# Optimization experiments

Measured on AMD Instinct MI355X. Metric: run time of the kernel, lower is better.

Reference implementation:

```python
import jax, jax.numpy as jnp
import numpy as np

D_MODEL = 1024
NUM_HEADS = 16
WINDOW = 128
DEPTH = D_MODEL // NUM_HEADS


def setup_inputs() -> dict:
    key = jax.random.key(0)
    ks = jax.random.split(key, 9)
    B, S = 2, 2048
    scale = 1.0 / np.sqrt(D_MODEL)
    x = jax.random.normal(ks[0], (B, S, D_MODEL), dtype=jnp.float32)
    Wq = jax.random.normal(ks[1], (D_MODEL, D_MODEL), dtype=jnp.float32) * scale
    Wk = jax.random.normal(ks[2], (D_MODEL, D_MODEL), dtype=jnp.float32) * scale
    Wv = jax.random.normal(ks[3], (D_MODEL, D_MODEL), dtype=jnp.float32) * scale
    Wo = jax.random.normal(ks[4], (D_MODEL, D_MODEL), dtype=jnp.float32) * scale
    bq = jnp.zeros((D_MODEL,), jnp.float32)
    bk = jnp.zeros((D_MODEL,), jnp.float32)
    bv = jnp.zeros((D_MODEL,), jnp.float32)
    bo = jnp.zeros((D_MODEL,), jnp.float32)
    return {"x": x, "Wq": Wq, "bq": bq, "Wk": Wk, "bk": bk,
            "Wv": Wv, "bv": bv, "Wo": Wo, "bo": bo}


def _split_heads(t, B, S):
    # [B,S,D] -> [B,H,S,depth]
    return t.reshape(B, S, NUM_HEADS, DEPTH).transpose(0, 2, 1, 3)


def reference(x, Wq, bq, Wk, bk, Wv, bv, Wo, bo):
    B, S, _ = x.shape
    q = _split_heads(x @ Wq + bq, B, S)
    k = _split_heads(x @ Wk + bk, B, S)
    v = _split_heads(x @ Wv + bv, B, S)
    scores = jnp.einsum('bhqd,bhkd->bhqk', q, k) / jnp.sqrt(jnp.float32(DEPTH))
    idx = jnp.arange(S)
    # mask[i_row=j, i_col=i] per original: |i - j| <= window (symmetric)
    local = jnp.abs(idx[None, :] - idx[:, None]) <= WINDOW  # [S,S]
    scores = jnp.where(local[None, None], scores, jnp.float32(-1e9))
    attn = jax.nn.softmax(scores, axis=-1)
    out = jnp.einsum('bhqk,bhkd->bhqd', attn, v)
    concat = out.transpose(0, 2, 1, 3).reshape(B, S, D_MODEL)
    return concat @ Wo + bo
```

## Files before the change

kernel.cpp:

```cpp
#include <hip/hip_runtime.h>
#include <cstdint>
#include <cstddef>

typedef __attribute__((ext_vector_type(8))) short short8;
typedef __attribute__((ext_vector_type(4))) short short4v;
typedef __attribute__((ext_vector_type(4))) float f32x4;
typedef short8 bf16x8;

typedef __attribute__((address_space(1))) const unsigned GU;
typedef __attribute__((address_space(3))) unsigned LU;

__device__ __forceinline__ short f2bf(float f) {
  unsigned u = __builtin_bit_cast(unsigned, f);
  u += 0x7fffu + ((u >> 16) & 1u);
  return (short)(u >> 16);
}

__global__ __launch_bounds__(256) void k_prep(const float* __restrict__ x,
                                              const float* __restrict__ W0, const float* __restrict__ W1,
                                              const float* __restrict__ W2, const float* __restrict__ W3,
                                              short* __restrict__ xb, short* __restrict__ WT) {
  __shared__ short T[64 * 72];
  int bid = blockIdx.x;
  int tid = threadIdx.x;
  if (bid < 2048) {
    size_t i = ((size_t)bid * 256 + tid) * 8;
    f32x4 a = *(const f32x4*)(x + i);
    f32x4 b = *(const f32x4*)(x + i + 4);
    short8 o;
#pragma unroll
    for (int j = 0; j < 4; ++j) { o[j] = f2bf(a[j]); o[4 + j] = f2bf(b[j]); }
    *(short8*)(xb + i) = o;
    return;
  }
  bid -= 2048;
  int widx = bid >> 8;
  int t = bid & 255;
  int kr = (t >> 4) * 64, nc = (t & 15) * 64;
  const float* W = widx == 0 ? W0 : widx == 1 ? W1 : widx == 2 ? W2 : W3;
  short* out = WT + (size_t)widx * 1048576;
#pragma unroll
  for (int i = 0; i < 4; ++i) {
    int idx = tid + i * 256;
    int k = idx >> 4, n4 = (idx & 15) << 2;
    f32x4 v = *(const f32x4*)(W + (size_t)(kr + k) * 1024 + nc + n4);
#pragma unroll
    for (int j = 0; j < 4; ++j) T[(n4 + j) * 72 + k] = f2bf(v[j]);
  }
  __syncthreads();
#pragma unroll
  for (int i = 0; i < 2; ++i) {
    int idx = tid + i * 256;
    int n = idx >> 3, k8 = (idx & 7) << 3;
    *(short8*)(out + (size_t)(nc + n) * 1024 + kr + k8) = *(const short8*)&T[n * 72 + k8];
  }
}

__global__ __launch_bounds__(512, 1) void k_gemm256(
    const short* __restrict__ A, const short* __restrict__ BT,
    const float* __restrict__ bias0, const float* __restrict__ bias1, const float* __restrict__ bias2,
    short* __restrict__ outb) {
  __shared__ short S[57344];
  const int tid = threadIdx.x;
  const int lane = tid & 63, w = tid >> 6;
  const int g = lane >> 4, qi = lane & 15;
  const int wm = w >> 2, wn = w & 3;
  int bid = blockIdx.x;
  int xcd = bid & 7, ii = bid >> 3;
  const int tm = (xcd >> 1) * 4 + (ii >> 3);
  const int tn = (xcd & 1) * 8 + (ii & 7);
  const int m0 = tm * 256, n0 = tn * 192;
  const size_t K = 1024;
  const short* Ab = A + (size_t)m0 * K;
  const short* Bb = BT + (size_t)n0 * K;

  auto stage64 = [&](int roff, const short* gbase, int kt) {
    int r = tid >> 3;
    int js = ((tid & 7) ^ (r & 7)) << 3;
    __builtin_amdgcn_global_load_lds((GU*)(gbase + (size_t)r * K + kt * 64 + js),
                                     (LU*)(&S[roff + tid * 8]), 16, 0, 0);
  };
  auto lda_a = [&](int bbase, int mf, int kk) -> bf16x8 {
    int row = (mf & 3) * 16 + qi;
    int reg = wm * 2 + (mf >> 2);
    return *(const bf16x8*)&S[bbase + reg * 4096 + row * 64 + (((kk * 4 + g) ^ (row & 7)) << 3)];
  };
  auto lda_b = [&](int bbase, int nf, int kk) -> bf16x8 {
    int c = wn * 48 + nf * 16 + qi;
    int reg = c >> 6, row = c & 63;
    return *(const bf16x8*)&S[bbase + 16384 + reg * 4096 + row * 64 + (((kk * 4 + g) ^ (row & 7)) << 3)];
  };

  f32x4 acc[8][3];
#pragma unroll
  for (int i = 0; i < 8; ++i)
#pragma unroll
    for (int j = 0; j < 3; ++j) acc[i][j] = (f32x4)(0.0f);

#define MFA(mi, ni, av, bv) \
  acc[mi][ni] = __builtin_amdgcn_mfma_f32_16x16x32_bf16(av, bv, acc[mi][ni], 0, 0, 0)
#define MF12(Aa, Bb_, o) \
  MFA((o)+0,0,(Aa)[(o)+0],(Bb_)[0]); MFA((o)+0,1,(Aa)[(o)+0],(Bb_)[1]); MFA((o)+0,2,(Aa)[(o)+0],(Bb_)[2]); \
  MFA((o)+1,0,(Aa)[(o)+1],(Bb_)[0]); MFA((o)+1,1,(Aa)[(o)+1],(Bb_)[1]); MFA((o)+1,2,(Aa)[(o)+1],(Bb_)[2]); \
  MFA((o)+2,0,(Aa)[(o)+2],(Bb_)[0]); MFA((o)+2,1,(Aa)[(o)+2],(Bb_)[1]); MFA((o)+2,2,(Aa)[(o)+2],(Bb_)[2]); \
  MFA((o)+3,0,(Aa)[(o)+3],(Bb_)[0]); MFA((o)+3,1,(Aa)[(o)+3],(Bb_)[1]); MFA((o)+3,2,(Aa)[(o)+3],(Bb_)[2])
#define SB __builtin_amdgcn_sched_barrier(0)
#define PHASE_TAIL(MFMAS) do { \
    SB; \
    __builtin_amdgcn_s_barrier(); \
    asm volatile("s_waitcnt lgkmcnt(0)" ::: "memory"); \
    SB; \
    __builtin_amdgcn_s_setprio(1); \
    MFMAS; \
    __builtin_amdgcn_s_setprio(0); \
    SB; \
    __builtin_amdgcn_s_barrier(); \
  } while (0)

  stage64(0,     Ab,            0);
  stage64(4096,  Ab + 65536,    0);
  stage64(8192,  Ab + 131072,   0);
  stage64(12288, Ab + 196608,   0);
  stage64(16384, Bb,            0);
  stage64(20480, Bb + 65536,    0);
  stage64(24576, Bb + 131072,   0);
  stage64(28672 + 16384, Bb,          1);
  stage64(28672 + 20480, Bb + 65536,  1);
  stage64(28672 + 24576, Bb + 131072, 1);
  asm volatile("s_waitcnt vmcnt(3)" ::: "memory");
  __builtin_amdgcn_s_barrier();

  for (int t = 0; t < 16; ++t) {
    const int b = t & 1, nb = b ^ 1;
    const int bb = b * 28672, nbb = nb * 28672;
    const int t1 = t + 1 < 15 ? t + 1 : 15;
    const int t2 = t + 2 < 15 ? t + 2 : 15;
    bf16x8 aA[8], aB[3], cA[8], cB[3];

#pragma unroll
    for (int mf = 0; mf < 4; ++mf) aA[mf] = lda_a(bb, mf, 0);
#pragma unroll
    for (int nf = 0; nf < 3; ++nf) aB[nf] = lda_b(bb, nf, 0);
    stage64(nbb,        Ab,         t1);
    stage64(nbb + 4096, Ab + 65536, t1);
    PHASE_TAIL(MF12(aA, aB, 0));
#pragma unroll
    for (int mf = 4; mf < 8; ++mf) aA[mf] = lda_a(bb, mf, 0);
#pragma unroll
    for (int nf = 0; nf < 3; ++nf) cB[nf] = lda_b(bb, nf, 1);
    stage64(nbb + 8192,  Ab + 131072, t1);
    stage64(nbb + 12288, Ab + 196608, t1);
    PHASE_TAIL(MF12(aA, aB, 4));
#pragma unroll
    for (int mf = 0; mf < 4; ++mf) cA[mf] = lda_a(bb, mf, 1);
    stage64(bb + 16384, Bb,         t2);
    stage64(bb + 20480, Bb + 65536, t2);
    PHASE_TAIL(MF12(cA, cB, 0));
#pragma unroll
    for (int mf = 4; mf < 8; ++mf) cA[mf] = lda_a(bb, mf, 1);
    stage64(bb + 24576, Bb + 131072, t2);
    asm volatile("s_waitcnt vmcnt(3)" ::: "memory");
    PHASE_TAIL(MF12(cA, cB, 4));
  }
#undef PHASE_TAIL
#undef MF12
#undef MFA
#undef SB

  asm volatile("s_waitcnt vmcnt(0)" ::: "memory");
  __syncthreads();
  float bv[3];
#pragma unroll
  for (int nf = 0; nf < 3; ++nf) {
    int colg = n0 + wn * 48 + nf * 16 + qi;
    int sel = colg >> 10;
    const float* bias = sel == 0 ? bias0 : (sel == 1 ? bias1 : bias2);
    bv[nf] = bias[colg & 1023];
  }
  short* Ep = S;
#pragma unroll
  for (int p = 0; p < 2; ++p) {
    __syncthreads();
    if (wm == p) {
#pragma unroll
      for (int mf = 0; mf < 8; ++mf)
#pragma unroll
        for (int nf = 0; nf < 3; ++nf)
#pragma unroll
          for (int j = 0; j < 4; ++j)
            Ep[(mf * 16 + g * 4 + j) * 200 + wn * 48 + nf * 16 + qi] =
                f2bf(acc[mf][nf][j] + bv[nf]);
    }
    __syncthreads();
#pragma unroll
    for (int i = 0; i < 6; ++i) {
      int idx = tid + i * 512;
      int r = idx / 24, c8 = (idx % 24) * 8;
      int grow = m0 + p * 128 + r;
      int colg = n0 + c8;
      int sel = colg >> 10;
      *(short8*)&outb[(size_t)sel * 4194304 + (size_t)grow * 1024 + (colg & 1023)] =
          *(const short8*)&Ep[r * 200 + c8];
    }
  }
}

__global__ __launch_bounds__(256, 2) void k_gemmO(
    const short* __restrict__ A, const short* __restrict__ BT,
    const float* __restrict__ bias0, float* __restrict__ outf) {
  __shared__ short Smem[16384];
  const int tid = threadIdx.x;
  const int lane = tid & 63, w = tid >> 6;
  const int g = lane >> 4, qi = lane & 15;
  const int wr = (w >> 1) * 64, wc = (w & 1) * 64;
  int bid = blockIdx.x;
  int xcd = bid & 7, ii = bid >> 3;
  const int tm = (xcd >> 1) * 8 + (ii >> 2);
  const int tn = (xcd & 1) * 4 + (ii & 3);
  const int m0 = tm * 128, n0 = tn * 128;
  const size_t K = 1024;
  const short* Ab = A + (size_t)m0 * K;
  const short* Bb = BT + (size_t)n0 * K;

  auto stage = [&](int buf, int k0) {
    short* Asb = Smem + buf * 4096;
    short* Bsb = Smem + 8192 + buf * 4096;
#pragma unroll
    for (int i = 0; i < 2; ++i) {
      int cidx = tid + i * 256;
      int r = cidx >> 2;
      int csw = ((cidx & 3) ^ ((r >> 1) & 3)) << 3;
      __builtin_amdgcn_global_load_lds((GU*)(Ab + (size_t)r * K + k0 + csw),
                                       (LU*)(&Asb[cidx * 8]), 16, 0, 0);
      __builtin_amdgcn_global_load_lds((GU*)(Bb + (size_t)r * K + k0 + csw),
                                       (LU*)(&Bsb[cidx * 8]), 16, 0, 0);
    }
  };

  f32x4 acc[4][4];
#pragma unroll
  for (int i = 0; i < 4; ++i)
#pragma unroll
    for (int j = 0; j < 4; ++j) acc[i][j] = (f32x4)(0.0f);

  stage(0, 0);
  __syncthreads();
  for (int kt = 0; kt < 32; ++kt) {
    int cur = kt & 1;
    if (kt < 31) stage(cur ^ 1, (kt + 1) * 32);
    const short* Asb = Smem + cur * 4096;
    const short* Bsb = Smem + 8192 + cur * 4096;
    bf16x8 a[4], b[4];
#pragma unroll
    for (int mf = 0; mf < 4; ++mf) {
      int R = wr + mf * 16 + qi;
      a[mf] = *(const bf16x8*)&Asb[R * 32 + ((g ^ ((R >> 1) & 3)) << 3)];
    }
#pragma unroll
    for (int nf = 0; nf < 4; ++nf) {
      int R = wc + nf * 16 + qi;
      b[nf] = *(const bf16x8*)&Bsb[R * 32 + ((g ^ ((R >> 1) & 3)) << 3)];
    }
#pragma unroll
    for (int mf = 0; mf < 4; ++mf)
#pragma unroll
      for (int nf = 0; nf < 4; ++nf)
        acc[mf][nf] = __builtin_amdgcn_mfma_f32_16x16x32_bf16(a[mf], b[nf], acc[mf][nf], 0, 0, 0);
    __syncthreads();
  }

  float* Ft = (float*)Smem;
  float bv[4];
#pragma unroll
  for (int nf = 0; nf < 4; ++nf) bv[nf] = bias0[n0 + wc + nf * 16 + qi];
#pragma unroll
  for (int mf = 0; mf < 4; ++mf) {
    __syncthreads();
#pragma unroll
    for (int nf = 0; nf < 4; ++nf)
#pragma unroll
      for (int j = 0; j < 4; ++j)
        Ft[((w >> 1) * 16 + g * 4 + j) * 136 + wc + nf * 16 + qi] = acc[mf][nf][j] + bv[nf];
    __syncthreads();
#pragma unroll
    for (int i = 0; i < 4; ++i) {
      int idx = tid + i * 256;
      int r = idx >> 5, c4 = (idx & 31) << 2;
      int row = m0 + ((r >> 4) << 6) + mf * 16 + (r & 15);
      *(f32x4*)&outf[(size_t)row * 1024 + n0 + c4] = *(const f32x4*)&Ft[r * 136 + c4];
    }
  }
}

__global__ __launch_bounds__(256, 2) void k_attn(const short* __restrict__ qg_,
                                                 const short* __restrict__ kg_,
                                                 const short* __restrict__ vg_,
                                                 short* __restrict__ outp) {
  __shared__ short Qs[64 * 72];
  __shared__ short Ks[64 * 72];
  __shared__ short Vs[64 * 72];
  __shared__ short Ps[4][16 * 72];
  int bid = blockIdx.x;
  int qt = bid & 31, h = (bid >> 5) & 15, b = bid >> 9;
  int q0 = qt * 64;
  int tid = threadIdx.x, lane = tid & 63, w = tid >> 6;
  int g = lane >> 4, qi = lane & 15;

  const short* qsrc = qg_ + ((size_t)b * 2048 + q0) * 1024 + h * 64;
#pragma unroll
  for (int i = 0; i < 2; ++i) {
    int idx = tid + i * 256;
    int r = idx >> 3, c = (idx & 7) << 3;
    *(short8*)&Qs[r * 72 + c] = *(const short8*)&qsrc[(size_t)r * 1024 + c];
  }
  __syncthreads();
  bf16x8 qf0 = *(const bf16x8*)&Qs[(w * 16 + qi) * 72 + g * 8];
  bf16x8 qf1 = *(const bf16x8*)&Qs[(w * 16 + qi) * 72 + 32 + g * 8];

  float m = -1e30f, l = 0.f;
  f32x4 oacc[4];
#pragma unroll
  for (int i = 0; i < 4; ++i) oacc[i] = (f32x4)(0.0f);
  int qglob = q0 + w * 16 + qi;

  for (int cc = 0; cc < 5; ++cc) {
    int kb0 = q0 - 128 + cc * 64;
    if (kb0 < 0 || kb0 >= 2048) continue;
    __syncthreads();
    const short* ksrc = kg_ + ((size_t)b * 2048 + kb0) * 1024 + h * 64;
    const short* vsrc = vg_ + ((size_t)b * 2048 + kb0) * 1024 + h * 64;
#pragma unroll
    for (int i = 0; i < 2; ++i) {
      int idx = tid + i * 256;
      int r = idx >> 3, c = (idx & 7) << 3;
      *(short8*)&Ks[r * 72 + c] = *(const short8*)&ksrc[(size_t)r * 1024 + c];
      short8 vv = *(const short8*)&vsrc[(size_t)r * 1024 + c];
#pragma unroll
      for (int j = 0; j < 8; ++j) {
        int d = c + j;
        Vs[d * 72 + ((r + ((d >> 3) << 3)) & 63)] = vv[j];
      }
    }
    __syncthreads();

    f32x4 st[4];
#pragma unroll
    for (int i = 0; i < 4; ++i) st[i] = (f32x4)(0.0f);
#pragma unroll
    for (int mf = 0; mf < 4; ++mf) {
      bf16x8 kf0 = *(const bf16x8*)&Ks[(mf * 16 + qi) * 72 + g * 8];
      bf16x8 kf1 = *(const bf16x8*)&Ks[(mf * 16 + qi) * 72 + 32 + g * 8];
      st[mf] = __builtin_amdgcn_mfma_f32_16x16x32_bf16(kf0, qf0, st[mf], 0, 0, 0);
      st[mf] = __builtin_amdgcn_mfma_f32_16x16x32_bf16(kf1, qf1, st[mf], 0, 0, 0);
    }

    float pv[16];
    float pm = -1e30f;
    if (cc >= 1 && cc <= 3) {
#pragma unroll
      for (int mf = 0; mf < 4; ++mf)
#pragma unroll
        for (int j = 0; j < 4; ++j) {
          float s = st[mf][j] * 0.125f;
          pv[mf * 4 + j] = s;
          pm = fmaxf(pm, s);
        }
    } else {
#pragma unroll
      for (int mf = 0; mf < 4; ++mf)
#pragma unroll
        for (int j = 0; j < 4; ++j) {
          int kcol = kb0 + mf * 16 + g * 4 + j;
          float s = st[mf][j] * 0.125f;
          int d = kcol - qglob;
          bool valid = (d >= -128) && (d <= 128);
          s = valid ? s : -1e30f;
          pv[mf * 4 + j] = s;
          pm = fmaxf(pm, s);
        }
    }
    pm = fmaxf(pm, __shfl_xor(pm, 16));
    pm = fmaxf(pm, __shfl_xor(pm, 32));
    float mnew = fmaxf(m, pm);
    float scale = __expf(m - mnew);
    float ls = 0.f;
#pragma unroll
    for (int e = 0; e < 16; ++e) {
      float p = pv[e] > -1e29f ? __expf(pv[e] - mnew) : 0.f;
      pv[e] = p;
      ls += p;
    }
    ls += __shfl_xor(ls, 16);
    ls += __shfl_xor(ls, 32);
    l = l * scale + ls;
    m = mnew;
#pragma unroll
    for (int mf = 0; mf < 4; ++mf) oacc[mf] *= scale;

#pragma unroll
    for (int f = 0; f < 4; ++f) {
      short4v pk;
#pragma unroll
      for (int j = 0; j < 4; ++j) pk[j] = f2bf(pv[f * 4 + j]);
      *(short4v*)&Ps[w][qi * 72 + f * 16 + g * 4] = pk;
    }

#pragma unroll
    for (int ks = 0; ks < 2; ++ks) {
      bf16x8 pf = *(const bf16x8*)&Ps[w][qi * 72 + ks * 32 + g * 8];
#pragma unroll
      for (int mf = 0; mf < 4; ++mf) {
        int dd = mf * 16 + qi;
        int pc = ((ks * 32 + g * 8) + ((dd >> 3) << 3)) & 63;
        bf16x8 vf = *(const bf16x8*)&Vs[dd * 72 + pc];
        oacc[mf] = __builtin_amdgcn_mfma_f32_16x16x32_bf16(vf, pf, oacc[mf], 0, 0, 0);
      }
    }
  }

  __syncthreads();
  short* Os = Ks;
  float inv = 1.f / l;
#pragma unroll
  for (int mf = 0; mf < 4; ++mf) {
    short4v pk;
#pragma unroll
    for (int j = 0; j < 4; ++j) pk[j] = f2bf(oacc[mf][j] * inv);
    *(short4v*)&Os[(w * 16 + qi) * 72 + mf * 16 + g * 4] = pk;
  }
  __syncthreads();
  short* dst = outp + ((size_t)b * 2048 + q0) * 1024 + h * 64;
  int r = tid >> 2, c16 = (tid & 3) << 4;
  *(short8*)&dst[(size_t)r * 1024 + c16] = *(const short8*)&Os[r * 72 + c16];
  *(short8*)&dst[(size_t)r * 1024 + c16 + 8] = *(const short8*)&Os[r * 72 + c16 + 8];
}

extern "C" void kernel_launch(void* const* d_in, const int* in_sizes, int n_in,
                              void* d_out, int out_size, void* d_ws, size_t ws_size,
                              hipStream_t stream) {
  const float* x  = (const float*)d_in[0];
  const float* Wq = (const float*)d_in[1];
  const float* bq = (const float*)d_in[2];
  const float* Wk = (const float*)d_in[3];
  const float* bk = (const float*)d_in[4];
  const float* Wv = (const float*)d_in[5];
  const float* bv = (const float*)d_in[6];
  const float* Wo = (const float*)d_in[7];
  const float* bo = (const float*)d_in[8];

  short* ws = (short*)d_ws;
  short* xb       = ws;
  short* qkv      = ws + 4194304;
  short* vbuf     = qkv + 2 * 4194304;
  short* attn_out = ws;
  short* WT       = ws + 4 * 4194304;

  k_prep<<<3072, 256, 0, stream>>>(x, Wq, Wk, Wv, Wo, xb, WT);
  k_gemm256<<<256, 512, 0, stream>>>(xb, WT, bq, bk, bv, qkv);
  k_attn<<<1024, 256, 0, stream>>>(qkv, qkv + 4194304, vbuf, attn_out);
  k_gemmO<<<256, 256, 0, stream>>>(attn_out, WT + 3 * 1048576, bo, (float*)d_out);
}
```

Measured before the change: 82.18 us.

## Triple-buffer A tiles in the projection GEMM to prefetch two steps ahead

```diff
diff --git a/kernel.cpp b/kernel.cpp
--- a/kernel.cpp
+++ b/kernel.cpp
@@ -60,7 +60,7 @@
     const short* __restrict__ A, const short* __restrict__ BT,
     const float* __restrict__ bias0, const float* __restrict__ bias1, const float* __restrict__ bias2,
     short* __restrict__ outb) {
-  __shared__ short S[57344];
+  __shared__ short S[73728];
   const int tid = threadIdx.x;
   const int lane = tid & 63, w = tid >> 6;
   const int g = lane >> 4, qi = lane & 15;
@@ -80,15 +80,15 @@
     __builtin_amdgcn_global_load_lds((GU*)(gbase + (size_t)r * K + kt * 64 + js),
                                      (LU*)(&S[roff + tid * 8]), 16, 0, 0);
   };
-  auto lda_a = [&](int bbase, int mf, int kk) -> bf16x8 {
+  auto lda_a = [&](int abase, int mf, int kk) -> bf16x8 {
     int row = (mf & 3) * 16 + qi;
     int reg = wm * 2 + (mf >> 2);
-    return *(const bf16x8*)&S[bbase + reg * 4096 + row * 64 + (((kk * 4 + g) ^ (row & 7)) << 3)];
+    return *(const bf16x8*)&S[abase + reg * 4096 + row * 64 + (((kk * 4 + g) ^ (row & 7)) << 3)];
   };
   auto lda_b = [&](int bbase, int nf, int kk) -> bf16x8 {
     int c = wn * 48 + nf * 16 + qi;
     int reg = c >> 6, row = c & 63;
-    return *(const bf16x8*)&S[bbase + 16384 + reg * 4096 + row * 64 + (((kk * 4 + g) ^ (row & 7)) << 3)];
+    return *(const bf16x8*)&S[bbase + reg * 4096 + row * 64 + (((kk * 4 + g) ^ (row & 7)) << 3)];
   };
 
   f32x4 acc[8][3];
@@ -117,49 +117,53 @@
     __builtin_amdgcn_s_barrier(); \
   } while (0)
 
-  stage64(0,     Ab,            0);
-  stage64(4096,  Ab + 65536,    0);
-  stage64(8192,  Ab + 131072,   0);
-  stage64(12288, Ab + 196608,   0);
-  stage64(16384, Bb,            0);
-  stage64(20480, Bb + 65536,    0);
-  stage64(24576, Bb + 131072,   0);
-  stage64(28672 + 16384, Bb,          1);
-  stage64(28672 + 20480, Bb + 65536,  1);
-  stage64(28672 + 24576, Bb + 131072, 1);
-  asm volatile("s_waitcnt vmcnt(3)" ::: "memory");
+  stage64(0,             Ab,            0);
+  stage64(4096,          Ab + 65536,    0);
+  stage64(8192,          Ab + 131072,   0);
+  stage64(12288,         Ab + 196608,   0);
+  stage64(49152,         Bb,            0);
+  stage64(49152 + 4096,  Bb + 65536,    0);
+  stage64(49152 + 8192,  Bb + 131072,   0);
+  stage64(16384,         Ab,            1);
+  stage64(16384 + 4096,  Ab + 65536,    1);
+  stage64(16384 + 8192,  Ab + 131072,   1);
+  stage64(16384 + 12288, Ab + 196608,   1);
+  stage64(61440,         Bb,            1);
+  stage64(61440 + 4096,  Bb + 65536,    1);
+  stage64(61440 + 8192,  Bb + 131072,   1);
+  asm volatile("s_waitcnt vmcnt(7)" ::: "memory");
   __builtin_amdgcn_s_barrier();
 
   for (int t = 0; t < 16; ++t) {
-    const int b = t & 1, nb = b ^ 1;
-    const int bb = b * 28672, nbb = nb * 28672;
-    const int t1 = t + 1 < 15 ? t + 1 : 15;
+    const int rA = (t % 3) * 16384;
+    const int a2 = ((t + 2) % 3) * 16384;
+    const int rB = 49152 + (t & 1) * 12288;
     const int t2 = t + 2 < 15 ? t + 2 : 15;
     bf16x8 aA[8], aB[3], cA[8], cB[3];
 
 #pragma unroll
-    for (int mf = 0; mf < 4; ++mf) aA[mf] = lda_a(bb, mf, 0);
-#pragma unroll
-    for (int nf = 0; nf < 3; ++nf) aB[nf] = lda_b(bb, nf, 0);
-    stage64(nbb,        Ab,         t1);
-    stage64(nbb + 4096, Ab + 65536, t1);
+    for (int mf = 0; mf < 4; ++mf) aA[mf] = lda_a(rA, mf, 0);
+#pragma unroll
+    for (int nf = 0; nf < 3; ++nf) aB[nf] = lda_b(rB, nf, 0);
+    stage64(a2,        Ab,         t2);
+    stage64(a2 + 4096, Ab + 65536, t2);
     PHASE_TAIL(MF12(aA, aB, 0));
 #pragma unroll
-    for (int mf = 4; mf < 8; ++mf) aA[mf] = lda_a(bb, mf, 0);
-#pragma unroll
-    for (int nf = 0; nf < 3; ++nf) cB[nf] = lda_b(bb, nf, 1);
-    stage64(nbb + 8192,  Ab + 131072, t1);
-    stage64(nbb + 12288, Ab + 196608, t1);
+    for (int mf = 4; mf < 8; ++mf) aA[mf] = lda_a(rA, mf, 0);
+#pragma unroll
+    for (int nf = 0; nf < 3; ++nf) cB[nf] = lda_b(rB, nf, 1);
+    stage64(a2 + 8192,  Ab + 131072, t2);
+    stage64(a2 + 12288, Ab + 196608, t2);
     PHASE_TAIL(MF12(aA, aB, 4));
 #pragma unroll
-    for (int mf = 0; mf < 4; ++mf) cA[mf] = lda_a(bb, mf, 1);
-    stage64(bb + 16384, Bb,         t2);
-    stage64(bb + 20480, Bb + 65536, t2);
+    for (int mf = 0; mf < 4; ++mf) cA[mf] = lda_a(rA, mf, 1);
+    stage64(rB,        Bb,         t2);
+    stage64(rB + 4096, Bb + 65536, t2);
     PHASE_TAIL(MF12(cA, cB, 0));
 #pragma unroll
-    for (int mf = 4; mf < 8; ++mf) cA[mf] = lda_a(bb, mf, 1);
-    stage64(bb + 24576, Bb + 131072, t2);
-    asm volatile("s_waitcnt vmcnt(3)" ::: "memory");
+    for (int mf = 4; mf < 8; ++mf) cA[mf] = lda_a(rA, mf, 1);
+    stage64(rB + 8192, Bb + 131072, t2);
+    asm volatile("s_waitcnt vmcnt(7)" ::: "memory");
     PHASE_TAIL(MF12(cA, cB, 4));
   }
 #undef PHASE_TAIL
```

After: 82.24 us. Within noise of the previous version (+0.1%).
